# Optimization experiments

Measured on AMD Instinct MI355X. Metric: run time of the kernel, lower is better.

Reference implementation:

```python
import jax, jax.numpy as jnp
import numpy as np

W0, W1 = 8, 8           # attn_grid_window_size
HEADS = 8
ATTN_CH = 256
HD = ATTN_CH // HEADS   # 32
LN_EPS = 1e-5
L2_EPS = 1e-12


def _rel_pos_index(h, w):
    # Swin-style relative position index, [h*w, h*w] int
    coords = np.stack(np.meshgrid(np.arange(h), np.arange(w), indexing='ij'))  # [2,h,w]
    coords = coords.reshape(2, -1)                                             # [2,L]
    rel = coords[:, :, None] - coords[:, None, :]                              # [2,L,L]
    rel = rel.transpose(1, 2, 0).astype(np.int64)                              # [L,L,2]
    rel[:, :, 0] += h - 1
    rel[:, :, 1] += w - 1
    rel[:, :, 0] *= 2 * w - 1
    return rel.sum(-1)                                                         # [L,L]

_REL_IDX = _rel_pos_index(W0, W1)


def _layernorm2d(x, g, b):
    # nn.LayerNorm((8,8)): normalize over the last two dims, affine shape (8,8)
    mu = jnp.mean(x, axis=(-2, -1), keepdims=True)
    var = jnp.var(x, axis=(-2, -1), keepdims=True)
    return (x - mu) * jax.lax.rsqrt(var + LN_EPS) * g + b


def setup_inputs() -> dict:
    key = jax.random.key(0)
    ks = jax.random.split(key, 8)
    C = 256
    return {
        'X': jax.random.normal(ks[0], (8, C, 128, 128), jnp.float32),
        'pre_gamma': jnp.ones((W0, W1), jnp.float32),
        'pre_beta': jnp.zeros((W0, W1), jnp.float32),
        'post_gamma': jnp.ones((W0, W1), jnp.float32),
        'post_beta': jnp.zeros((W0, W1), jnp.float32),
        'Wqkv': jax.random.normal(ks[1], (3 * ATTN_CH, C), jnp.float32) * 0.02,
        'bqkv': jnp.zeros((3 * ATTN_CH,), jnp.float32),
        'Wproj': jax.random.normal(ks[2], (C, ATTN_CH), jnp.float32) * 0.02,
        'bproj': jnp.zeros((C,), jnp.float32),
        'rel_bias_table': jax.random.normal(ks[3], ((2 * W0 - 1) * (2 * W1 - 1), HEADS), jnp.float32) * 0.02,
    }


def reference(X, pre_gamma, pre_beta, post_gamma, post_beta,
              Wqkv, bqkv, Wproj, bproj, rel_bias_table):
    N, C, H, W = X.shape
    L = W0 * W1
    # --- block partition (mirrors torch view/permute/contiguous().view) ---
    xp = X.reshape(N, C, H // W0, W0, W // W1, W1)
    xp = xp.transpose(0, 2, 4, 3, 5, 1).reshape(-1, C, W0, W1)  # [Bw, C, 8, 8]
    Bw = xp.shape[0]
    # --- pre-norm over the window dims ---
    xn = _layernorm2d(xp, pre_gamma, pre_beta)
    # --- windowed multi-head self-attention with relative position bias ---
    x = xn.reshape(Bw, C, L)
    qkv = jnp.einsum('oc,bcl->bol', Wqkv, x) + bqkv[None, :, None]   # [Bw, 3A, L]
    qkv = qkv.reshape(Bw, 3, HEADS, HD, L)
    q = qkv[:, 0].transpose(0, 1, 3, 2)  # [Bw, h, L, d]
    k = qkv[:, 1].transpose(0, 1, 3, 2)
    v = qkv[:, 2].transpose(0, 1, 3, 2)
    # MetNet-3 qk normalization (L2 normalize instead of 1/sqrt(d) scale)
    q = q / jnp.clip(jnp.linalg.norm(q, axis=-1, keepdims=True), L2_EPS)
    k = k / jnp.clip(jnp.linalg.norm(k, axis=-1, keepdims=True), L2_EPS)
    bias = rel_bias_table[jnp.asarray(_REL_IDX)].transpose(2, 0, 1)  # [h, L, L]
    attn = jnp.einsum('bhld,bhmd->bhlm', q, k) + bias[None]          # [Bw, h, L, L]
    attn = jax.nn.softmax(attn, axis=-1)
    out = jnp.einsum('bhlm,bhmd->bhld', attn, v)                     # [Bw, h, L, d]
    out = out.transpose(0, 1, 3, 2).reshape(Bw, ATTN_CH, L)          # [Bw, A, L]
    out = jnp.einsum('ca,bal->bcl', Wproj, out) + bproj[None, :, None]
    out = out.reshape(Bw, C, W0, W1)
    # --- residual, post-norm + Identity MLP residual ---
    y = xp + out
    y = y + _layernorm2d(y, post_gamma, post_beta)
    # --- reverse partition: composition of torch .view()s == plain reshape ---
    return y.reshape(N, C, H, W)
```

## Files before the change

### kernel.cpp

```cpp
#include <hip/hip_runtime.h>

typedef __bf16 bf16x8 __attribute__((ext_vector_type(8)));
typedef float  f32x4  __attribute__((ext_vector_type(4)));
typedef unsigned short ushort4v __attribute__((ext_vector_type(4)));

#define DEVI static __device__ __forceinline__

DEVI unsigned short f2bf(float f) {
  union { float f; unsigned u; } v; v.f = f;
  unsigned u = v.u;
  u += 0x7fffu + ((u >> 16) & 1u);
  return (unsigned short)(u >> 16);
}
DEVI float bf2f(unsigned short s) {
  union { unsigned u; float f; } v; v.u = ((unsigned)s) << 16;
  return v.f;
}

__global__ void prep_kernel(const float* __restrict__ Wqkv, const float* __restrict__ Wproj,
                            const float* __restrict__ table,
                            unsigned short* __restrict__ wq, unsigned short* __restrict__ wp,
                            float* __restrict__ biasg, float* __restrict__ rowsum) {
  const int i = blockIdx.x * 256 + threadIdx.x;
  if (i < 768 * 256) wq[i] = f2bf(Wqkv[i]);
  if (i < 256 * 256) wp[i] = f2bf(Wproj[i]);
  if (i < 8 * 64 * 64) {
    const int h = i >> 12, r = (i >> 6) & 63, c = i & 63;
    const int ridx = ((r >> 3) - (c >> 3) + 7) * 15 + ((r & 7) - (c & 7) + 7);
    biasg[i] = table[ridx * 8 + h];
  }
  if (i < 768) {
    const float4* p = reinterpret_cast<const float4*>(Wqkv + (size_t)i * 256);
    float s = 0.f;
#pragma unroll
    for (int j = 0; j < 64; ++j) { const float4 a = p[j]; s += a.x + a.y + a.z + a.w; }
    rowsum[i] = s;
  }
}

#define LDS_XN 0u
#define LDS_ST 32768u
#define LDS_Q  34816u
#define LDS_K  75776u
#define LDS_V  116736u
#define LDS_XW 34816u
#define LDS_YO 75776u
#define LDS_TOTAL 149504u

__global__ void __launch_bounds__(512, 2)
win_attn_kernel(const float* __restrict__ X,
                const float* __restrict__ preg, const float* __restrict__ preb,
                const float* __restrict__ postg, const float* __restrict__ postb,
                const float* __restrict__ bqkv, const float* __restrict__ bproj,
                const unsigned short* __restrict__ wq, const unsigned short* __restrict__ wp,
                const float* __restrict__ biasg, const float* __restrict__ rowsum,
                float* __restrict__ out) {
  __shared__ alignas(16) unsigned char sh[LDS_TOTAL];
  const int tid = threadIdx.x;
  const int w = tid >> 6;
  const int lane = tid & 63, lm = lane & 15, lg = lane >> 4;
  const int orig = blockIdx.x;
  const int b = (orig & 7) * 256 + (orig >> 3);
  const int n = b >> 8, gh = (b >> 4) & 15, gw = b & 15;
  const size_t wbase = (size_t)n * 4194304 + (size_t)gh * 1024 + (size_t)gw * 8;

  {
#pragma unroll
    for (int i = 0; i < 4; ++i) {
      const int rid = i * 512 + tid;
      const int cc = rid >> 3, w0 = rid & 7;
      const float* xb = X + wbase + (size_t)cc * 16384 + w0 * 128;
      const float4 a  = *reinterpret_cast<const float4*>(xb);
      const float4 bv = *reinterpret_cast<const float4*>(xb + 4);
      const unsigned xorv = (cc & 64) ? 16u : 0u;
      unsigned char* dst = sh + LDS_XW + (unsigned)cc * 272u + (unsigned)w0 * 32u;
      *reinterpret_cast<float4*>(dst + xorv)         = a;
      *reinterpret_cast<float4*>(dst + (16u ^ xorv)) = bv;
    }
  }
  __syncthreads();

  {
    const int c = tid >> 1, half = tid & 1;
    const int r = ((c >> 5) << 3) + ((c >> 2) & 7);
    const unsigned base = LDS_XW + (unsigned)(c & 3) * (64u * 272u)
                        + 4u * (unsigned)(r ^ ((c & 1) << 2));
    float fv[32];
    float s1 = 0.f, s2 = 0.f;
#pragma unroll
    for (int i = 0; i < 32; ++i) {
      const int l = half * 32 + i;
      const float v = *reinterpret_cast<const float*>(sh + base + (unsigned)l * 272u);
      fv[i] = v; s1 += v; s2 += v * v;
    }
    s1 += __shfl_xor(s1, 1);
    s2 += __shfl_xor(s2, 1);
    const float mean = s1 * (1.f / 64.f);
    float var = s2 * (1.f / 64.f) - mean * mean;
    var = fmaxf(var, 0.f) + 1e-5f;
    const float rstd = rsqrtf(var);
    const float sig  = var * rstd;
#pragma unroll
    for (int i = 0; i < 32; ++i) {
      const int l = half * 32 + i;
      *(unsigned short*)(sh + LDS_XN + l * 512 +
          (((unsigned)(2 * c)) ^ ((unsigned)((l & 7) << 4)))) = f2bf((fv[i] - mean) * rstd);
    }
    if (!half) *reinterpret_cast<float2*>(sh + LDS_ST + c * 8) = float2{mean, sig};
  }
  __syncthreads();

  {
    float pg4[4], pb4[4];
#pragma unroll
    for (int nt = 0; nt < 4; ++nt) { pg4[nt] = preg[nt * 16 + lm]; pb4[nt] = preb[nt * 16 + lm]; }
    const int wbase96 = w * 96;
    f32x4 acc[6][4];
#pragma unroll
    for (int i = 0; i < 6; ++i)
#pragma unroll
      for (int j = 0; j < 4; ++j) acc[i][j] = f32x4{0.f, 0.f, 0.f, 0.f};
    for (int ks = 0; ks < 8; ++ks) {
      bf16x8 bfrag[4];
#pragma unroll
      for (int nt = 0; nt < 4; ++nt) {
        const int l = nt * 16 + lm;
        bfrag[nt] = *reinterpret_cast<const bf16x8*>(
            sh + LDS_XN + l * 512 + (((unsigned)(ks * 64 + lg * 16)) ^ ((unsigned)((l & 7) << 4))));
      }
#pragma unroll
      for (int m4 = 0; m4 < 6; ++m4) {
        const int o = wbase96 + m4 * 16 + lm;
        const bf16x8 a = *reinterpret_cast<const bf16x8*>(
            (const unsigned char*)wq + ((size_t)o * 512 + ks * 64 + lg * 16));
#pragma unroll
        for (int nt = 0; nt < 4; ++nt)
          acc[m4][nt] = __builtin_amdgcn_mfma_f32_16x16x32_bf16(a, bfrag[nt], acc[m4][nt], 0, 0, 0);
      }
    }
    f32x4 rs4[6], bq4[6];
#pragma unroll
    for (int m4 = 0; m4 < 6; ++m4) {
      rs4[m4] = *reinterpret_cast<const f32x4*>(rowsum + wbase96 + m4 * 16 + lg * 4);
      bq4[m4] = *reinterpret_cast<const f32x4*>(bqkv   + wbase96 + m4 * 16 + lg * 4);
    }
#pragma unroll
    for (int m4 = 0; m4 < 6; ++m4) {
      const int ob = wbase96 + m4 * 16;
      if (ob < 512) {
        const unsigned qkbase = (ob < 256) ? LDS_Q : LDS_K;
        const int o0 = (ob & 255) + lg * 4;
        const int h = o0 >> 5, d0 = o0 & 31;
#pragma unroll
        for (int nt = 0; nt < 4; ++nt) {
          const int l = nt * 16 + lm;
          ushort4v pk;
#pragma unroll
          for (int reg = 0; reg < 4; ++reg)
            pk[reg] = f2bf(pg4[nt] * acc[m4][nt][reg] + pb4[nt] * rs4[m4][reg] + bq4[m4][reg]);
          *reinterpret_cast<ushort4v*>(sh + qkbase + h * 5120 + l * 80 + 2 * d0) = pk;
        }
      } else {
        const int o20 = ob - 512 + lg * 4;
#pragma unroll
        for (int reg = 0; reg < 4; ++reg) {
          const int o2 = o20 + reg;
          const int h = o2 >> 5, d = o2 & 31;
          const float rs = rs4[m4][reg], bq = bq4[m4][reg];
#pragma unroll
          for (int nt = 0; nt < 4; ++nt) {
            const int l = nt * 16 + lm;
            *(unsigned short*)(sh + LDS_V + h * 4096 + d * 128 +
                (((unsigned)(2 * l)) ^ ((unsigned)((d & 7) << 4)))) =
                f2bf(pg4[nt] * acc[m4][nt][reg] + pb4[nt] * rs + bq);
          }
        }
      }
    }
  }
  __syncthreads();

  {
#pragma unroll
    for (int j = 0; j < 2; ++j) {
      const unsigned base = j ? LDS_K : LDS_Q;
      const int h = tid >> 6, l = tid & 63;
      unsigned* row = (unsigned*)(sh + base + h * 5120 + l * 80);
      unsigned u[16];
      float ss = 0.f;
#pragma unroll
      for (int t2 = 0; t2 < 16; ++t2) {
        u[t2] = row[t2];
        const float lo = bf2f((unsigned short)(u[t2] & 0xffffu));
        const float hi = bf2f((unsigned short)(u[t2] >> 16));
        ss += lo * lo + hi * hi;
      }
      const float inv = 1.f / fmaxf(sqrtf(ss), 1e-12f);
#pragma unroll
      for (int t2 = 0; t2 < 16; ++t2) {
        const float lo = bf2f((unsigned short)(u[t2] & 0xffffu)) * inv;
        const float hi = bf2f((unsigned short)(u[t2] >> 16)) * inv;
        row[t2] = (unsigned)f2bf(lo) | (((unsigned)f2bf(hi)) << 16);
      }
    }
  }
  __syncthreads();

  {
    const int h = w;
    const unsigned pbase = LDS_Q + (unsigned)w * 8192u;
    bf16x8 qf[4], kf[4];
#pragma unroll
    for (int mt = 0; mt < 4; ++mt)
      qf[mt] = *reinterpret_cast<const bf16x8*>(sh + LDS_Q + h * 5120 + (mt * 16 + lm) * 80 + lg * 16);
#pragma unroll
    for (int nt = 0; nt < 4; ++nt)
      kf[nt] = *reinterpret_cast<const bf16x8*>(sh + LDS_K + h * 5120 + (nt * 16 + lm) * 80 + lg * 16);
    __syncthreads();

    const float* bh = biasg + h * 4096;
    float p[4][4][4];
#pragma unroll
    for (int mt = 0; mt < 4; ++mt)
#pragma unroll
      for (int reg = 0; reg < 4; ++reg) {
        const int rrow = mt * 16 + lg * 4 + reg;
#pragma unroll
        for (int nt = 0; nt < 4; ++nt)
          p[mt][nt][reg] = bh[rrow * 64 + nt * 16 + lm];
      }

    f32x4 s[4][4];
#pragma unroll
    for (int nt = 0; nt < 4; ++nt)
#pragma unroll
      for (int mt = 0; mt < 4; ++mt)
        s[mt][nt] = __builtin_amdgcn_mfma_f32_16x16x32_bf16(qf[mt], kf[nt], f32x4{0.f,0.f,0.f,0.f}, 0, 0, 0);

    float rinv[4][4];
#pragma unroll
    for (int mt = 0; mt < 4; ++mt)
#pragma unroll
      for (int reg = 0; reg < 4; ++reg) {
        float m = -1e30f;
#pragma unroll
        for (int nt = 0; nt < 4; ++nt) {
          const float v = s[mt][nt][reg] + p[mt][nt][reg];
          p[mt][nt][reg] = v;
          m = fmaxf(m, v);
        }
        m = fmaxf(m, __shfl_xor(m, 1));
        m = fmaxf(m, __shfl_xor(m, 2));
        m = fmaxf(m, __shfl_xor(m, 4));
        m = fmaxf(m, __shfl_xor(m, 8));
        float sum = 0.f;
#pragma unroll
        for (int nt = 0; nt < 4; ++nt) {
          const float e = __expf(p[mt][nt][reg] - m);
          p[mt][nt][reg] = e;
          sum += e;
        }
        sum += __shfl_xor(sum, 1);
        sum += __shfl_xor(sum, 2);
        sum += __shfl_xor(sum, 4);
        sum += __shfl_xor(sum, 8);
        rinv[mt][reg] = 1.f / sum;
      }
#pragma unroll
    for (int mt = 0; mt < 4; ++mt)
#pragma unroll
      for (int reg = 0; reg < 4; ++reg) {
        const int rrow = mt * 16 + lg * 4 + reg;
#pragma unroll
        for (int nt = 0; nt < 4; ++nt) {
          const int ccol = nt * 16 + lm;
          *(unsigned short*)(sh + pbase + rrow * 128 +
              (((unsigned)(2 * ccol)) ^ ((unsigned)((rrow & 7) << 4)))) = f2bf(p[mt][nt][reg] * rinv[mt][reg]);
        }
      }
    f32x4 oacc[4][2];
#pragma unroll
    for (int mt = 0; mt < 4; ++mt) { oacc[mt][0] = f32x4{0.f,0.f,0.f,0.f}; oacc[mt][1] = f32x4{0.f,0.f,0.f,0.f}; }
#pragma unroll
    for (int ks = 0; ks < 2; ++ks) {
      bf16x8 pa[4];
#pragma unroll
      for (int mt = 0; mt < 4; ++mt) {
        const int l = mt * 16 + lm;
        pa[mt] = *reinterpret_cast<const bf16x8*>(
            sh + pbase + l * 128 + (((unsigned)(ks * 64 + lg * 16)) ^ ((unsigned)((l & 7) << 4))));
      }
#pragma unroll
      for (int nt = 0; nt < 2; ++nt) {
        const int d = nt * 16 + lm;
        const bf16x8 vf = *reinterpret_cast<const bf16x8*>(
            sh + LDS_V + h * 4096 + d * 128 + (((unsigned)(ks * 64 + lg * 16)) ^ ((unsigned)((d & 7) << 4))));
#pragma unroll
        for (int mt = 0; mt < 4; ++mt)
          oacc[mt][nt] = __builtin_amdgcn_mfma_f32_16x16x32_bf16(pa[mt], vf, oacc[mt][nt], 0, 0, 0);
      }
    }
    __syncthreads();
#pragma unroll
    for (int mt = 0; mt < 4; ++mt)
#pragma unroll
      for (int reg = 0; reg < 4; ++reg) {
        const int l = mt * 16 + lg * 4 + reg;
#pragma unroll
        for (int nt = 0; nt < 2; ++nt) {
          const int d = nt * 16 + lm;
          *(unsigned short*)(sh + LDS_Q + h * 5120 + l * 80 + 2 * d) = f2bf(oacc[mt][nt][reg]);
        }
      }
  }
  __syncthreads();

  {
    float pog4[4], pob4[4];
#pragma unroll
    for (int nt = 0; nt < 4; ++nt) { pog4[nt] = postg[nt * 16 + lm]; pob4[nt] = postb[nt * 16 + lm]; }
    f32x4 acc[2][4];
#pragma unroll
    for (int i = 0; i < 2; ++i)
#pragma unroll
      for (int j = 0; j < 4; ++j) acc[i][j] = f32x4{0.f, 0.f, 0.f, 0.f};
    for (int ks = 0; ks < 8; ++ks) {
      bf16x8 bfr[4];
#pragma unroll
      for (int nt = 0; nt < 4; ++nt) {
        const int l = nt * 16 + lm;
        bfr[nt] = *reinterpret_cast<const bf16x8*>(sh + LDS_Q + (unsigned)ks * 5120 + l * 80 + lg * 16);
      }
#pragma unroll
      for (int mt = 0; mt < 2; ++mt) {
        const int c = w * 32 + mt * 16 + lm;
        const bf16x8 a = *reinterpret_cast<const bf16x8*>(
            (const unsigned char*)wp + ((size_t)c * 512 + ks * 64 + lg * 16));
#pragma unroll
        for (int nt = 0; nt < 4; ++nt)
          acc[mt][nt] = __builtin_amdgcn_mfma_f32_16x16x32_bf16(a, bfr[nt], acc[mt][nt], 0, 0, 0);
      }
    }
#pragma unroll
    for (int mt = 0; mt < 2; ++mt) {
      const float4 bp4 = *reinterpret_cast<const float4*>(bproj + w * 32 + mt * 16 + lg * 4);
#pragma unroll
      for (int reg = 0; reg < 4; ++reg) {
        const int c = w * 32 + mt * 16 + lg * 4 + reg;
        const float bp = ((const float*)&bp4)[reg];
        const float2 ms = *reinterpret_cast<const float2*>(sh + LDS_ST + c * 8);
        float y[4];
        float s1 = 0.f, s2 = 0.f;
#pragma unroll
        for (int nt = 0; nt < 4; ++nt) {
          const int l = nt * 16 + lm;
          const float xh = bf2f(*(const unsigned short*)(
              sh + LDS_XN + l * 512 + (((unsigned)(2 * c)) ^ ((unsigned)((l & 7) << 4)))));
          const float v = xh * ms.y + ms.x + acc[mt][nt][reg] + bp;
          y[nt] = v;
          s1 += v; s2 += v * v;
        }
        s1 += __shfl_xor(s1, 1); s2 += __shfl_xor(s2, 1);
        s1 += __shfl_xor(s1, 2); s2 += __shfl_xor(s2, 2);
        s1 += __shfl_xor(s1, 4); s2 += __shfl_xor(s2, 4);
        s1 += __shfl_xor(s1, 8); s2 += __shfl_xor(s2, 8);
        const float mean = s1 * (1.f / 64.f);
        const float var  = s2 * (1.f / 64.f) - mean * mean;
        const float rstd = rsqrtf(fmaxf(var, 0.f) + 1e-5f);
#pragma unroll
        for (int nt = 0; nt < 4; ++nt) {
          const int l = nt * 16 + lm;
          const float v = y[nt];
          *reinterpret_cast<float*>(sh + LDS_YO + (unsigned)c * 256u +
              (((unsigned)(4 * l)) ^ ((unsigned)((c & 1) << 6)))) =
              v + (v - mean) * rstd * pog4[nt] + pob4[nt];
        }
      }
    }
  }
  __syncthreads();

  {
    const size_t ob = (size_t)b * 16384;
#pragma unroll
    for (int i = 0; i < 8; ++i) {
      const int flat = i * 512 + tid;
      const int c = flat >> 4, ch = flat & 15;
      const float4 v = *reinterpret_cast<const float4*>(
          sh + LDS_YO + (unsigned)c * 256u + (((unsigned)(ch * 16)) ^ ((unsigned)((c & 1) << 6))));
      *reinterpret_cast<float4*>(out + ob + (size_t)flat * 4) = v;
    }
  }
}

extern "C" void kernel_launch(void* const* d_in, const int* in_sizes, int n_in,
                              void* d_out, int out_size, void* d_ws, size_t ws_size,
                              hipStream_t stream) {
  const float* X     = (const float*)d_in[0];
  const float* preg  = (const float*)d_in[1];
  const float* preb  = (const float*)d_in[2];
  const float* postg = (const float*)d_in[3];
  const float* postb = (const float*)d_in[4];
  const float* Wqkv  = (const float*)d_in[5];
  const float* bqkv  = (const float*)d_in[6];
  const float* Wproj = (const float*)d_in[7];
  const float* bproj = (const float*)d_in[8];
  const float* table = (const float*)d_in[9];

  unsigned short* wq = (unsigned short*)d_ws;
  unsigned short* wp = (unsigned short*)((char*)d_ws + 393216);
  float* biasg       = (float*)((char*)d_ws + 524288);
  float* rowsum      = (float*)((char*)d_ws + 655360);

  prep_kernel<<<768, 256, 0, stream>>>(Wqkv, Wproj, table, wq, wp, biasg, rowsum);
  win_attn_kernel<<<2048, 512, 0, stream>>>(X, preg, preb, postg, postb,
                                            bqkv, bproj, wq, wp, biasg, rowsum,
                                            (float*)d_out);
}
```

Baseline: 307.1 us.

## Fuse qk L2-normalization into QKV epilogue and prefetch weight fragments

Moves the per-row L2 normalization of q and k into the QKV GEMM epilogue, computing it on fp32 accumulators with cross-lane shuffles. This removes a separate LDS read/modify/write pass and one barrier. The attention stage now loads V fragments early and stores P into the Q/K regions of its own head, which drops another barrier. Weight fragments for both GEMMs are software-prefetched one k-step ahead, and f2bf uses the native bf16 conversion. The trade-offs are higher register pressure and slightly different rounding, since q and k are normalized before the bf16 cast.

```diff
diff --git a/kernel.cpp b/kernel.cpp
--- a/kernel.cpp
+++ b/kernel.cpp
@@ -7,10 +7,8 @@
 #define DEVI static __device__ __forceinline__
 
 DEVI unsigned short f2bf(float f) {
-  union { float f; unsigned u; } v; v.f = f;
-  unsigned u = v.u;
-  u += 0x7fffu + ((u >> 16) & 1u);
-  return (unsigned short)(u >> 16);
+  __bf16 h = (__bf16)f;
+  return __builtin_bit_cast(unsigned short, h);
 }
 DEVI float bf2f(unsigned short s) {
   union { unsigned u; float f; } v; v.u = ((unsigned)s) << 16;
@@ -115,12 +113,24 @@
 #pragma unroll
     for (int nt = 0; nt < 4; ++nt) { pg4[nt] = preg[nt * 16 + lm]; pb4[nt] = preb[nt * 16 + lm]; }
     const int wbase96 = w * 96;
+    const unsigned char* abase = (const unsigned char*)wq + ((size_t)(wbase96 + lm) * 512 + lg * 16);
     f32x4 acc[6][4];
 #pragma unroll
     for (int i = 0; i < 6; ++i)
 #pragma unroll
       for (int j = 0; j < 4; ++j) acc[i][j] = f32x4{0.f, 0.f, 0.f, 0.f};
+    bf16x8 acur[6];
+#pragma unroll
+    for (int m4 = 0; m4 < 6; ++m4)
+      acur[m4] = *reinterpret_cast<const bf16x8*>(abase + m4 * 8192);
+#pragma unroll
     for (int ks = 0; ks < 8; ++ks) {
+      bf16x8 anxt[6];
+      if (ks < 7) {
+#pragma unroll
+        for (int m4 = 0; m4 < 6; ++m4)
+          anxt[m4] = *reinterpret_cast<const bf16x8*>(abase + m4 * 8192 + (ks + 1) * 64);
+      }
       bf16x8 bfrag[4];
 #pragma unroll
       for (int nt = 0; nt < 4; ++nt) {
@@ -129,95 +139,107 @@
             sh + LDS_XN + l * 512 + (((unsigned)(ks * 64 + lg * 16)) ^ ((unsigned)((l & 7) << 4))));
       }
 #pragma unroll
-      for (int m4 = 0; m4 < 6; ++m4) {
-        const int o = wbase96 + m4 * 16 + lm;
-        const bf16x8 a = *reinterpret_cast<const bf16x8*>(
-            (const unsigned char*)wq + ((size_t)o * 512 + ks * 64 + lg * 16));
+      for (int m4 = 0; m4 < 6; ++m4)
 #pragma unroll
         for (int nt = 0; nt < 4; ++nt)
-          acc[m4][nt] = __builtin_amdgcn_mfma_f32_16x16x32_bf16(a, bfrag[nt], acc[m4][nt], 0, 0, 0);
-      }
-    }
-    f32x4 rs4[6], bq4[6];
+          acc[m4][nt] = __builtin_amdgcn_mfma_f32_16x16x32_bf16(acur[m4], bfrag[nt], acc[m4][nt], 0, 0, 0);
+      if (ks < 7) {
+#pragma unroll
+        for (int m4 = 0; m4 < 6; ++m4) acur[m4] = anxt[m4];
+      }
+    }
 #pragma unroll
     for (int m4 = 0; m4 < 6; ++m4) {
-      rs4[m4] = *reinterpret_cast<const f32x4*>(rowsum + wbase96 + m4 * 16 + lg * 4);
-      bq4[m4] = *reinterpret_cast<const f32x4*>(bqkv   + wbase96 + m4 * 16 + lg * 4);
-    }
-#pragma unroll
-    for (int m4 = 0; m4 < 6; ++m4) {
-      const int ob = wbase96 + m4 * 16;
-      if (ob < 512) {
-        const unsigned qkbase = (ob < 256) ? LDS_Q : LDS_K;
-        const int o0 = (ob & 255) + lg * 4;
-        const int h = o0 >> 5, d0 = o0 & 31;
-#pragma unroll
-        for (int nt = 0; nt < 4; ++nt) {
-          const int l = nt * 16 + lm;
-          ushort4v pk;
-#pragma unroll
-          for (int reg = 0; reg < 4; ++reg)
-            pk[reg] = f2bf(pg4[nt] * acc[m4][nt][reg] + pb4[nt] * rs4[m4][reg] + bq4[m4][reg]);
-          *reinterpret_cast<ushort4v*>(sh + qkbase + h * 5120 + l * 80 + 2 * d0) = pk;
-        }
-      } else {
-        const int o20 = ob - 512 + lg * 4;
-#pragma unroll
-        for (int reg = 0; reg < 4; ++reg) {
-          const int o2 = o20 + reg;
-          const int h = o2 >> 5, d = o2 & 31;
-          const float rs = rs4[m4][reg], bq = bq4[m4][reg];
+      const f32x4 rs4 = *reinterpret_cast<const f32x4*>(rowsum + wbase96 + m4 * 16 + lg * 4);
+      const f32x4 bq4 = *reinterpret_cast<const f32x4*>(bqkv   + wbase96 + m4 * 16 + lg * 4);
+#pragma unroll
+      for (int nt = 0; nt < 4; ++nt)
+#pragma unroll
+        for (int reg = 0; reg < 4; ++reg)
+          acc[m4][nt][reg] = pg4[nt] * acc[m4][nt][reg] + pb4[nt] * rs4[reg] + bq4[reg];
+    }
+#pragma unroll
+    for (int hh = 0; hh < 3; ++hh) {
+      const int hh3 = w * 3 + hh;
+      if (hh3 < 16) {
+#pragma unroll
+        for (int nt = 0; nt < 4; ++nt) {
+          float ss = 0.f;
+#pragma unroll
+          for (int half = 0; half < 2; ++half)
+#pragma unroll
+            for (int reg = 0; reg < 4; ++reg) {
+              const float v = acc[2 * hh + half][nt][reg];
+              ss += v * v;
+            }
+          ss += __shfl_xor(ss, 16);
+          ss += __shfl_xor(ss, 32);
+          const float inv = 1.f / fmaxf(sqrtf(ss), 1e-12f);
+#pragma unroll
+          for (int half = 0; half < 2; ++half)
+#pragma unroll
+            for (int reg = 0; reg < 4; ++reg)
+              acc[2 * hh + half][nt][reg] *= inv;
+        }
+      }
+    }
+#pragma unroll
+    for (int hh = 0; hh < 3; ++hh) {
+      const int hh3 = w * 3 + hh;
+      if (hh3 < 16) {
+        const unsigned base = (hh3 < 8) ? (LDS_Q + (unsigned)hh3 * 5120u)
+                                        : (LDS_K + (unsigned)(hh3 - 8) * 5120u);
+#pragma unroll
+        for (int half = 0; half < 2; ++half) {
+          const int d0 = half * 16 + lg * 4;
 #pragma unroll
           for (int nt = 0; nt < 4; ++nt) {
             const int l = nt * 16 + lm;
-            *(unsigned short*)(sh + LDS_V + h * 4096 + d * 128 +
-                (((unsigned)(2 * l)) ^ ((unsigned)((d & 7) << 4)))) =
-                f2bf(pg4[nt] * acc[m4][nt][reg] + pb4[nt] * rs + bq);
+            ushort4v pk;
+#pragma unroll
+            for (int reg = 0; reg < 4; ++reg) pk[reg] = f2bf(acc[2 * hh + half][nt][reg]);
+            *reinterpret_cast<ushort4v*>(sh + base + l * 80 + 2 * d0) = pk;
           }
         }
+      } else {
+        const int hv = hh3 - 16;
+#pragma unroll
+        for (int half = 0; half < 2; ++half)
+#pragma unroll
+          for (int reg = 0; reg < 4; ++reg) {
+            const int d = half * 16 + lg * 4 + reg;
+#pragma unroll
+            for (int nt = 0; nt < 4; ++nt) {
+              const int l = nt * 16 + lm;
+              *(unsigned short*)(sh + LDS_V + hv * 4096 + d * 128 +
+                  (((unsigned)(2 * l)) ^ ((unsigned)((d & 7) << 4)))) =
+                  f2bf(acc[2 * hh + half][nt][reg]);
+            }
+          }
       }
     }
   }
   __syncthreads();
 
   {
-#pragma unroll
-    for (int j = 0; j < 2; ++j) {
-      const unsigned base = j ? LDS_K : LDS_Q;
-      const int h = tid >> 6, l = tid & 63;
-      unsigned* row = (unsigned*)(sh + base + h * 5120 + l * 80);
-      unsigned u[16];
-      float ss = 0.f;
-#pragma unroll
-      for (int t2 = 0; t2 < 16; ++t2) {
-        u[t2] = row[t2];
-        const float lo = bf2f((unsigned short)(u[t2] & 0xffffu));
-        const float hi = bf2f((unsigned short)(u[t2] >> 16));
-        ss += lo * lo + hi * hi;
-      }
-      const float inv = 1.f / fmaxf(sqrtf(ss), 1e-12f);
-#pragma unroll
-      for (int t2 = 0; t2 < 16; ++t2) {
-        const float lo = bf2f((unsigned short)(u[t2] & 0xffffu)) * inv;
-        const float hi = bf2f((unsigned short)(u[t2] >> 16)) * inv;
-        row[t2] = (unsigned)f2bf(lo) | (((unsigned)f2bf(hi)) << 16);
-      }
-    }
-  }
-  __syncthreads();
-
-  {
     const int h = w;
-    const unsigned pbase = LDS_Q + (unsigned)w * 8192u;
-    bf16x8 qf[4], kf[4];
+    const unsigned qh = LDS_Q + (unsigned)w * 5120u;
+    const unsigned kh = LDS_K + (unsigned)w * 5120u;
+    bf16x8 qf[4], kf[4], vf[2][2];
 #pragma unroll
     for (int mt = 0; mt < 4; ++mt)
-      qf[mt] = *reinterpret_cast<const bf16x8*>(sh + LDS_Q + h * 5120 + (mt * 16 + lm) * 80 + lg * 16);
+      qf[mt] = *reinterpret_cast<const bf16x8*>(sh + qh + (mt * 16 + lm) * 80 + lg * 16);
 #pragma unroll
     for (int nt = 0; nt < 4; ++nt)
-      kf[nt] = *reinterpret_cast<const bf16x8*>(sh + LDS_K + h * 5120 + (nt * 16 + lm) * 80 + lg * 16);
-    __syncthreads();
-
+      kf[nt] = *reinterpret_cast<const bf16x8*>(sh + kh + (nt * 16 + lm) * 80 + lg * 16);
+#pragma unroll
+    for (int ks = 0; ks < 2; ++ks)
+#pragma unroll
+      for (int nt = 0; nt < 2; ++nt) {
+        const int d = nt * 16 + lm;
+        vf[ks][nt] = *reinterpret_cast<const bf16x8*>(
+            sh + LDS_V + h * 4096 + d * 128 + (((unsigned)(ks * 64 + lg * 16)) ^ ((unsigned)((d & 7) << 4))));
+      }
     const float* bh = biasg + h * 4096;
     float p[4][4][4];
 #pragma unroll
@@ -229,14 +251,12 @@
         for (int nt = 0; nt < 4; ++nt)
           p[mt][nt][reg] = bh[rrow * 64 + nt * 16 + lm];
       }
-
     f32x4 s[4][4];
 #pragma unroll
     for (int nt = 0; nt < 4; ++nt)
 #pragma unroll
       for (int mt = 0; mt < 4; ++mt)
         s[mt][nt] = __builtin_amdgcn_mfma_f32_16x16x32_bf16(qf[mt], kf[nt], f32x4{0.f,0.f,0.f,0.f}, 0, 0, 0);
-
     float rinv[4][4];
 #pragma unroll
     for (int mt = 0; mt < 4; ++mt)
@@ -274,8 +294,10 @@
 #pragma unroll
         for (int nt = 0; nt < 4; ++nt) {
           const int ccol = nt * 16 + lm;
-          *(unsigned short*)(sh + pbase + rrow * 128 +
-              (((unsigned)(2 * ccol)) ^ ((unsigned)((rrow & 7) << 4)))) = f2bf(p[mt][nt][reg] * rinv[mt][reg]);
+          const unsigned flat = (unsigned)(rrow * 128) +
+              (((unsigned)(2 * ccol)) ^ ((unsigned)((rrow & 7) << 4)));
+          const unsigned addr = (flat < 5120u) ? (qh + flat) : (kh + flat - 5120u);
+          *(unsigned short*)(sh + addr) = f2bf(p[mt][nt][reg] * rinv[mt][reg]);
         }
       }
     f32x4 oacc[4][2];
@@ -287,20 +309,17 @@
 #pragma unroll
       for (int mt = 0; mt < 4; ++mt) {
         const int l = mt * 16 + lm;
-        pa[mt] = *reinterpret_cast<const bf16x8*>(
-            sh + pbase + l * 128 + (((unsigned)(ks * 64 + lg * 16)) ^ ((unsigned)((l & 7) << 4))));
-      }
-#pragma unroll
-      for (int nt = 0; nt < 2; ++nt) {
-        const int d = nt * 16 + lm;
-        const bf16x8 vf = *reinterpret_cast<const bf16x8*>(
-            sh + LDS_V + h * 4096 + d * 128 + (((unsigned)(ks * 64 + lg * 16)) ^ ((unsigned)((d & 7) << 4))));
+        const unsigned flat = (unsigned)(l * 128) +
+            (((unsigned)(ks * 64 + lg * 16)) ^ ((unsigned)((l & 7) << 4)));
+        const unsigned addr = (flat < 5120u) ? (qh + flat) : (kh + flat - 5120u);
+        pa[mt] = *reinterpret_cast<const bf16x8*>(sh + addr);
+      }
+#pragma unroll
+      for (int nt = 0; nt < 2; ++nt)
 #pragma unroll
         for (int mt = 0; mt < 4; ++mt)
-          oacc[mt][nt] = __builtin_amdgcn_mfma_f32_16x16x32_bf16(pa[mt], vf, oacc[mt][nt], 0, 0, 0);
-      }
-    }
-    __syncthreads();
+          oacc[mt][nt] = __builtin_amdgcn_mfma_f32_16x16x32_bf16(pa[mt], vf[ks][nt], oacc[mt][nt], 0, 0, 0);
+    }
 #pragma unroll
     for (int mt = 0; mt < 4; ++mt)
 #pragma unroll
@@ -309,7 +328,7 @@
 #pragma unroll
         for (int nt = 0; nt < 2; ++nt) {
           const int d = nt * 16 + lm;
-          *(unsigned short*)(sh + LDS_Q + h * 5120 + l * 80 + 2 * d) = f2bf(oacc[mt][nt][reg]);
+          *(unsigned short*)(sh + qh + l * 80 + 2 * d) = f2bf(oacc[mt][nt][reg]);
         }
       }
   }
@@ -319,12 +338,24 @@
     float pog4[4], pob4[4];
 #pragma unroll
     for (int nt = 0; nt < 4; ++nt) { pog4[nt] = postg[nt * 16 + lm]; pob4[nt] = postb[nt * 16 + lm]; }
+    const unsigned char* abase = (const unsigned char*)wp + ((size_t)(w * 32 + lm) * 512 + lg * 16);
     f32x4 acc[2][4];
 #pragma unroll
     for (int i = 0; i < 2; ++i)
 #pragma unroll
       for (int j = 0; j < 4; ++j) acc[i][j] = f32x4{0.f, 0.f, 0.f, 0.f};
+    bf16x8 acur[2];
+#pragma unroll
+    for (int mt = 0; mt < 2; ++mt)
+      acur[mt] = *reinterpret_cast<const bf16x8*>(abase + mt * 8192);
+#pragma unroll
     for (int ks = 0; ks < 8; ++ks) {
+      bf16x8 anxt[2];
+      if (ks < 7) {
+#pragma unroll
+        for (int mt = 0; mt < 2; ++mt)
+          anxt[mt] = *reinterpret_cast<const bf16x8*>(abase + mt * 8192 + (ks + 1) * 64);
+      }
       bf16x8 bfr[4];
 #pragma unroll
       for (int nt = 0; nt < 4; ++nt) {
@@ -332,13 +363,13 @@
         bfr[nt] = *reinterpret_cast<const bf16x8*>(sh + LDS_Q + (unsigned)ks * 5120 + l * 80 + lg * 16);
       }
 #pragma unroll
-      for (int mt = 0; mt < 2; ++mt) {
-        const int c = w * 32 + mt * 16 + lm;
-        const bf16x8 a = *reinterpret_cast<const bf16x8*>(
-            (const unsigned char*)wp + ((size_t)c * 512 + ks * 64 + lg * 16));
+      for (int mt = 0; mt < 2; ++mt)
 #pragma unroll
         for (int nt = 0; nt < 4; ++nt)
-          acc[mt][nt] = __builtin_amdgcn_mfma_f32_16x16x32_bf16(a, bfr[nt], acc[mt][nt], 0, 0, 0);
+          acc[mt][nt] = __builtin_amdgcn_mfma_f32_16x16x32_bf16(acur[mt], bfr[nt], acc[mt][nt], 0, 0, 0);
+      if (ks < 7) {
+#pragma unroll
+        for (int mt = 0; mt < 2; ++mt) acur[mt] = anxt[mt];
       }
     }
 #pragma unroll
```

After: 293.2 us. -4.5%, faster.
